# Kernel tuning notes

Measured on AMD Instinct MI355X. Metric: run time of the kernel, lower is better.

Reference implementation:

```python
import math
import jax, jax.numpy as jnp
import numpy as np

B, T, C, H = 4, 2048, 1024, 16
D = C // H  # head dim = 64


def setup_inputs() -> dict:
    key = jax.random.key(0)
    ks = jax.random.split(key, 9)
    s = 1.0 / math.sqrt(C)
    return {
        "x": jax.random.normal(ks[0], (B, T, C), jnp.float32),
        "Wq": jax.random.normal(ks[1], (C, C), jnp.float32) * s,
        "bq": jax.random.normal(ks[2], (C,), jnp.float32) * 0.02,
        "Wk": jax.random.normal(ks[3], (C, C), jnp.float32) * s,
        "bk": jax.random.normal(ks[4], (C,), jnp.float32) * 0.02,
        "Wv": jax.random.normal(ks[5], (C, C), jnp.float32) * s,
        "bv": jax.random.normal(ks[6], (C,), jnp.float32) * 0.02,
        "Wo": jax.random.normal(ks[7], (C, C), jnp.float32) * s,
        "bo": jax.random.normal(ks[8], (C,), jnp.float32) * 0.02,
    }


def reference(x, Wq, bq, Wk, bk, Wv, bv, Wo, bo):
    # Projections: (B,T,C) -> (B,H,T,D)
    def heads(y):
        return y.reshape(B, T, H, D).transpose(0, 2, 1, 3)

    q = heads(x @ Wq + bq)
    k = heads(x @ Wk + bk)
    v = heads(x @ Wv + bv)

    scale = 1.0 / math.sqrt(D)
    scores = jnp.einsum("bhqd,bhkd->bhqk", q, k) * scale  # (B,H,T,T)
    causal = jnp.tril(jnp.ones((T, T), dtype=bool))
    scores = jnp.where(causal[None, None], scores, jnp.float32(-jnp.inf))
    att = jax.nn.softmax(scores, axis=-1)

    y = jnp.einsum("bhqk,bhkd->bhqd", att, v)  # (B,H,T,D)
    y = y.transpose(0, 2, 1, 3).reshape(B, T, C)
    return y @ Wo + bo
```

## Files before the change

kernel.cpp:

```cpp
#include <hip/hip_runtime.h>

#define B_ 4
#define T_ 2048
#define C_ 1024
#define H_ 16
#define D_ 64
#define M_ (B_*T_)
#define CR3 3072

typedef unsigned short u16;
typedef __attribute__((ext_vector_type(8))) short short8;
typedef __attribute__((ext_vector_type(8))) unsigned short ushort8_t;
typedef __attribute__((ext_vector_type(4))) unsigned short ushort4_t;
typedef __attribute__((ext_vector_type(4))) float floatx4;
typedef __attribute__((ext_vector_type(16))) float f32x16;
typedef __attribute__((ext_vector_type(4))) unsigned int uint4_t;

__device__ __forceinline__ u16 f2bf(float f) {
  union { float f; unsigned u; } v; v.f = f;
  unsigned r = v.u + 0x7fffu + ((v.u >> 16) & 1u);
  return (u16)(r >> 16);
}

__device__ __forceinline__ void gload16(const void* g, void* l) {
  __builtin_amdgcn_global_load_lds((__attribute__((address_space(1))) void*)(g),
                                   (__attribute__((address_space(3))) void*)(l),
                                   16, 0, 0);
}

__device__ __forceinline__ unsigned cvtpk(float lo, float hi) {
  unsigned r;
  asm("v_cvt_pk_bf16_f32 %0, %1, %2" : "=v"(r) : "v"(lo), "v"(hi));
  return r;
}

__device__ __forceinline__ void pl32swap(unsigned &a, unsigned &b) {
  asm volatile("v_permlane32_swap_b32 %0, %1" : "+v"(a), "+v"(b));
}

#define MFMA32(a, b, c) __builtin_amdgcn_mfma_f32_32x32x16_bf16(a, b, c, 0, 0, 0)
#define MFMA16(a, b, c) __builtin_amdgcn_mfma_f32_16x16x32_bf16(a, b, c, 0, 0, 0)

__global__ __launch_bounds__(256) void convx_k(const float* __restrict__ x,
                                               u16* __restrict__ o) {
  int i = (blockIdx.x * 256 + threadIdx.x) * 4;
  floatx4 v = *(const floatx4*)(x + i);
  ushort4_t r;
#pragma unroll
  for (int j = 0; j < 4; ++j) r[j] = f2bf(v[j]);
  *(ushort4_t*)(o + i) = r;
}

__global__ __launch_bounds__(256) void wconv_k(const float* __restrict__ W0,
                                               const float* __restrict__ W1,
                                               const float* __restrict__ W2,
                                               const float* __restrict__ W3,
                                               u16* __restrict__ WT) {
  __shared__ float tile[64][65];
  const float* W = blockIdx.z == 0 ? W0 : blockIdx.z == 1 ? W1 : blockIdx.z == 2 ? W2 : W3;
  const float sc = blockIdx.z == 0 ? 0.125f * 1.44269504f : 1.0f;
  u16* Wt = WT + (size_t)blockIdx.z * (C_ * C_);
  int k0 = blockIdx.x * 64, n0 = blockIdx.y * 64;
  int t = threadIdx.x;
  int r = t >> 2, c0 = (t & 3) * 16;
#pragma unroll
  for (int j = 0; j < 4; ++j) {
    floatx4 v = *(const floatx4*)(W + (size_t)(k0 + r) * C_ + n0 + c0 + j * 4);
#pragma unroll
    for (int jj = 0; jj < 4; ++jj) tile[r][c0 + j * 4 + jj] = v[jj];
  }
  __syncthreads();
  ushort8_t o0, o1;
#pragma unroll
  for (int j = 0; j < 8; ++j) o0[j] = f2bf(tile[c0 + j][r] * sc);
#pragma unroll
  for (int j = 0; j < 8; ++j) o1[j] = f2bf(tile[c0 + 8 + j][r] * sc);
  *(ushort8_t*)(Wt + (size_t)(n0 + r) * C_ + k0 + c0) = o0;
  *(ushort8_t*)(Wt + (size_t)(n0 + r) * C_ + k0 + c0 + 8) = o1;
}

__global__ __launch_bounds__(256, 2) void gemm8_k(const u16* __restrict__ A,
                                                  const u16* __restrict__ Wt,
                                                  const float* __restrict__ b0,
                                                  const float* __restrict__ b1,
                                                  const float* __restrict__ b2,
                                                  float bsc0,
                                                  u16* __restrict__ Cout) {
  __shared__ u16 lds3[36864];
  const int tid = threadIdx.x;
  const int lane = tid & 63, wn = tid >> 6;
  const int l15 = lane & 15, g = lane >> 4;

  const int bid = blockIdx.x;
  const int swz = (bid & 7) * 96 + (bid >> 3);
  const int bn = swz >> 6, bm = swz & 63;
  const int m0 = bm * 128, n0 = bn * 256;

  const int srow = tid >> 2;
  const int scol = ((tid & 3) ^ ((srow >> 1) & 3)) * 8;
  const u16* gA = A  + (size_t)(m0 + srow) * 1024 + scol;
  const u16* gB = Wt + (size_t)(n0 + srow) * 1024 + scol;

#define STAGE(KT) do { \
    u16* s_ = lds3 + ((KT) % 3) * 12288; \
    gload16(gA + (KT) * 32,                      s_ + tid * 8); \
    gload16(gA + (size_t)64 * 1024 + (KT) * 32,  s_ + 2048 + tid * 8); \
    gload16(gB + (KT) * 32,                      s_ + 4096 + tid * 8); \
    gload16(gB + (size_t)64 * 1024 + (KT) * 32,  s_ + 6144 + tid * 8); \
    gload16(gB + (size_t)128 * 1024 + (KT) * 32, s_ + 8192 + tid * 8); \
    gload16(gB + (size_t)192 * 1024 + (KT) * 32, s_ + 10240 + tid * 8); \
  } while (0)

  floatx4 acc[8][4] = {};

  STAGE(0);
  STAGE(1);

  for (int kt = 0; kt < 32; ++kt) {
    if (kt < 31) asm volatile("s_waitcnt vmcnt(6)" ::: "memory");
    else         asm volatile("s_waitcnt vmcnt(0)" ::: "memory");
    __builtin_amdgcn_s_barrier();
    __builtin_amdgcn_sched_barrier(0);
    if (kt < 30) STAGE(kt + 2);

    const u16* Ab = lds3 + (kt % 3) * 12288;
    const u16* Bb = Ab + 4096;
    short8 af[8], bf[4];
#pragma unroll
    for (int mi = 0; mi < 8; ++mi) {
      int ra = mi * 16 + l15;
      af[mi] = *(const short8*)(Ab + ra * 32 + ((g ^ ((ra >> 1) & 3)) << 3));
    }
#pragma unroll
    for (int ni = 0; ni < 4; ++ni) {
      int rb = wn * 64 + ni * 16 + l15;
      bf[ni] = *(const short8*)(Bb + rb * 32 + ((g ^ ((rb >> 1) & 3)) << 3));
    }
    __builtin_amdgcn_s_setprio(1);
#pragma unroll
    for (int mi = 0; mi < 8; ++mi)
#pragma unroll
      for (int ni = 0; ni < 4; ++ni)
        acc[mi][ni] = MFMA16(af[mi], bf[ni], acc[mi][ni]);
    __builtin_amdgcn_s_setprio(0);
  }

#pragma unroll
  for (int mi = 0; mi < 8; ++mi) {
    int row = m0 + mi * 16 + g * 4;
#pragma unroll
    for (int ni = 0; ni < 4; ++ni) {
      int col = n0 + wn * 64 + ni * 16 + l15;
      int seg = col >> 10;
      const float* bp = seg == 0 ? b0 : seg == 1 ? b1 : b2;
      float bv = bp[col & 1023] * (seg == 0 ? bsc0 : 1.0f);
#pragma unroll
      for (int i = 0; i < 4; ++i)
        Cout[(size_t)(row + i) * CR3 + col] = f2bf(acc[mi][ni][i] + bv);
    }
  }
}

template <int OUTF32>
__global__ __launch_bounds__(256, 2) void gemm_k(const u16* __restrict__ A,
                                                 int astride,
                                                 const u16* __restrict__ Wt,
                                                 const float* __restrict__ b0,
                                                 void* __restrict__ Cout, int ostride) {
  __shared__ u16 As[128 * 32];
  __shared__ u16 Bs[128 * 32];
  const int tid = threadIdx.x;
  const int w = tid >> 6, lane = tid & 63;
  const int wr = (w >> 1) * 64, wc = (w & 1) * 64;
  const int l15 = lane & 15, g = lane >> 4;
  const int m0 = blockIdx.x * 128, n0 = blockIdx.y * 128;

  floatx4 acc[4][4] = {};

  const int srow = tid >> 2;
  const int scol = ((tid & 3) ^ ((srow >> 1) & 3)) * 8;
  const u16* ga = A + (size_t)(m0 + srow) * astride + scol;
  const u16* gb = Wt + (size_t)(n0 + srow) * C_ + scol;
  u16* lA = As + tid * 8;
  u16* lB = Bs + tid * 8;

  for (int kt = 0; kt < C_; kt += 32) {
    gload16(ga + kt, lA);
    gload16(ga + kt + (size_t)64 * astride, lA + 64 * 32);
    gload16(gb + kt, lB);
    gload16(gb + kt + (size_t)64 * C_, lB + 64 * 32);
    asm volatile("s_waitcnt vmcnt(0)" ::: "memory");
    __syncthreads();
    short8 af[4], bf[4];
#pragma unroll
    for (int i = 0; i < 4; ++i) {
      int ra = wr + i * 16 + l15;
      af[i] = *(const short8*)(As + ra * 32 + ((g ^ ((ra >> 1) & 3)) << 3));
    }
#pragma unroll
    for (int i = 0; i < 4; ++i) {
      int rb = wc + i * 16 + l15;
      bf[i] = *(const short8*)(Bs + rb * 32 + ((g ^ ((rb >> 1) & 3)) << 3));
    }
#pragma unroll
    for (int mi = 0; mi < 4; ++mi)
#pragma unroll
      for (int ni = 0; ni < 4; ++ni)
        acc[mi][ni] = MFMA16(af[mi], bf[ni], acc[mi][ni]);
    __syncthreads();
  }
#pragma unroll
  for (int mi = 0; mi < 4; ++mi) {
    int row = m0 + wr + mi * 16 + g * 4;
#pragma unroll
    for (int ni = 0; ni < 4; ++ni) {
      int col = n0 + wc + ni * 16 + l15;
      float bv = b0[col];
#pragma unroll
      for (int i = 0; i < 4; ++i) {
        float v = acc[mi][ni][i] + bv;
        if (OUTF32)
          ((float*)Cout)[(size_t)(row + i) * ostride + col] = v;
        else
          ((u16*)Cout)[(size_t)(row + i) * ostride + col] = f2bf(v);
      }
    }
  }
}

__global__ __launch_bounds__(256, 2) void attn_k(const u16* __restrict__ QKV,
                                                 u16* __restrict__ Yg) {
  __shared__ u16 Ks[2][64 * 64];
  __shared__ u16 Vt[2][64 * 64];

  const int tid = threadIdx.x;
  const int w = tid >> 6, lane = tid & 63;
  const int qi = lane & 31, h = lane >> 5;

  const int lid = blockIdx.x;
  const int a4 = lid >> 6;
  const int gq = a4 >> 2, iq = a4 & 3;
  const int jt = gq == 0 ? 15 - 2 * iq : gq == 1 ? 2 * iq : gq == 2 ? 14 - 2 * iq : 1 + 2 * iq;
  const int bh = lid & 63;
  const int nt = 2 * jt + 2;

  const size_t baseQ = (size_t)(bh >> 4) * T_ * CR3 + (size_t)(bh & 15) * D_;
  const size_t baseY = (size_t)(bh >> 4) * T_ * C_ + (size_t)(bh & 15) * D_;
  const u16* Kg = QKV + baseQ + 1024;
  const u16* Vg = QKV + baseQ + 2048;

  const int srow = tid >> 3, schunk = tid & 7;
  const int sgcol = (schunk ^ (srow & 7)) * 8;
  const u16* Kgr = Kg + (size_t)srow * CR3 + sgcol;
  const u16* Vgr = Vg + (size_t)srow * CR3 + schunk * 8;

  const int qw0 = 128 * jt + 32 * w;
  const int q_abs = qw0 + qi;

  short8 qf0, qf1, qf2, qf3;
  {
    const u16* Qr = QKV + baseQ + (size_t)q_abs * CR3 + 8 * h;
    qf0 = *(const short8*)(Qr);      qf1 = *(const short8*)(Qr + 16);
    qf2 = *(const short8*)(Qr + 32); qf3 = *(const short8*)(Qr + 48);
  }

  ushort8_t va, vbr;
  gload16(Kgr, &Ks[0][tid * 8]);
  gload16(Kgr + (size_t)32 * CR3, &Ks[0][2048 + tid * 8]);
  va = *(const ushort8_t*)(Vgr);
  vbr = *(const ushort8_t*)(Vgr + (size_t)32 * CR3);

  f32x16 y0 = {}, y1 = {};
  float l_run = 0.f;
  const float M0 = 13.0f;

  for (int t = 0; t < nt; ++t) {
    const int kv0 = t * 64;
    u16* Kb = Ks[t & 1];
    u16* Vb = Vt[t & 1];
    asm volatile("s_waitcnt vmcnt(0)" ::: "memory");
    {
      char* vbp = (char*)Vb;
#pragma unroll
      for (int j = 0; j < 8; ++j) {
        int d = schunk * 8 + j;
        int sl = ((schunk ^ j) & 7) << 4;
        *(u16*)(vbp + d * 128 + ((2 * srow) ^ sl)) = va[j];
        *(u16*)(vbp + d * 128 + ((2 * (srow + 32)) ^ sl)) = vbr[j];
      }
    }
    __syncthreads();
    if (t + 1 < nt) {
      int nkv = (t + 1) * 64;
      u16* dst = Ks[(t + 1) & 1];
      gload16(Kgr + (size_t)nkv * CR3, dst + tid * 8);
      gload16(Kgr + (size_t)(nkv + 32) * CR3, dst + 2048 + tid * 8);
      va = *(const ushort8_t*)(Vgr + (size_t)nkv * CR3);
      vbr = *(const ushort8_t*)(Vgr + (size_t)(nkv + 32) * CR3);
    }

    if (kv0 <= qw0 + 31) {
      f32x16 s0 = {}, s1 = {};
      {
        const int swq = (qi & 7) << 4;
        const char* kr0 = (const char*)Kb + qi * 128;
        const char* kr1 = (const char*)Kb + (qi + 32) * 128;
        short8 k0, k1;
        k0 = *(const short8*)(kr0 + ((16 * h) ^ swq));
        k1 = *(const short8*)(kr1 + ((16 * h) ^ swq));
        s0 = MFMA32(k0, qf0, s0); s1 = MFMA32(k1, qf0, s1);
        k0 = *(const short8*)(kr0 + ((32 + 16 * h) ^ swq));
        k1 = *(const short8*)(kr1 + ((32 + 16 * h) ^ swq));
        s0 = MFMA32(k0, qf1, s0); s1 = MFMA32(k1, qf1, s1);
        k0 = *(const short8*)(kr0 + ((64 + 16 * h) ^ swq));
        k1 = *(const short8*)(kr1 + ((64 + 16 * h) ^ swq));
        s0 = MFMA32(k0, qf2, s0); s1 = MFMA32(k1, qf2, s1);
        k0 = *(const short8*)(kr0 + ((96 + 16 * h) ^ swq));
        k1 = *(const short8*)(kr1 + ((96 + 16 * h) ^ swq));
        s0 = MFMA32(k0, qf3, s0); s1 = MFMA32(k1, qf3, s1);
      }
      if (kv0 + 63 > qw0) {
#pragma unroll
        for (int r = 0; r < 16; ++r) {
          int kvq = (r & 3) + 8 * (r >> 2) + 4 * h;
          if (kv0 + kvq > q_abs) s0[r] = -1e30f;
          if (kv0 + 32 + kvq > q_abs) s1[r] = -1e30f;
        }
      }
#pragma unroll
      for (int r = 0; r < 16; ++r) s0[r] = __builtin_amdgcn_exp2f(s0[r] - M0);
#pragma unroll
      for (int r = 0; r < 16; ++r) s1[r] = __builtin_amdgcn_exp2f(s1[r] - M0);
      {
        float a8[8];
#pragma unroll
        for (int r = 0; r < 8; ++r) a8[r] = (s0[r] + s0[r + 8]) + (s1[r] + s1[r + 8]);
#pragma unroll
        for (int r = 0; r < 4; ++r) a8[r] += a8[r + 4];
        l_run += (a8[0] + a8[1]) + (a8[2] + a8[3]);
      }
      unsigned pw[16];
      {
        unsigned a0, b0, a1, b1;
        a0 = cvtpk(s0[0], s0[1]);  b0 = cvtpk(s0[4], s0[5]);  pl32swap(a0, b0);
        a1 = cvtpk(s0[2], s0[3]);  b1 = cvtpk(s0[6], s0[7]);  pl32swap(a1, b1);
        pw[0] = a0; pw[1] = a1; pw[2] = b0; pw[3] = b1;
        a0 = cvtpk(s0[8], s0[9]);  b0 = cvtpk(s0[12], s0[13]); pl32swap(a0, b0);
        a1 = cvtpk(s0[10], s0[11]); b1 = cvtpk(s0[14], s0[15]); pl32swap(a1, b1);
        pw[4] = a0; pw[5] = a1; pw[6] = b0; pw[7] = b1;
        a0 = cvtpk(s1[0], s1[1]);  b0 = cvtpk(s1[4], s1[5]);  pl32swap(a0, b0);
        a1 = cvtpk(s1[2], s1[3]);  b1 = cvtpk(s1[6], s1[7]);  pl32swap(a1, b1);
        pw[8] = a0; pw[9] = a1; pw[10] = b0; pw[11] = b1;
        a0 = cvtpk(s1[8], s1[9]);  b0 = cvtpk(s1[12], s1[13]); pl32swap(a0, b0);
        a1 = cvtpk(s1[10], s1[11]); b1 = cvtpk(s1[14], s1[15]); pl32swap(a1, b1);
        pw[12] = a0; pw[13] = a1; pw[14] = b0; pw[15] = b1;
      }
      {
        const char* vb0 = (const char*)Vb + qi * 128;
        const char* vb1 = (const char*)Vb + (qi + 32) * 128;
        const int sx0 = (((qi >> 3) ^ qi) & 7) << 4;
        const int sx1 = sx0 ^ 0x40;
#pragma unroll
        for (int c = 0; c < 4; ++c) {
          int cb = 32 * c + 16 * h;
          uint4_t pt = {pw[c * 4 + 0], pw[c * 4 + 1], pw[c * 4 + 2], pw[c * 4 + 3]};
          short8 pa = __builtin_bit_cast(short8, pt);
          short8 v0 = *(const short8*)(vb0 + (cb ^ sx0));
          short8 v1 = *(const short8*)(vb1 + (cb ^ sx1));
          y0 = MFMA32(pa, v0, y0);
          y1 = MFMA32(pa, v1, y1);
        }
      }
    }
    __syncthreads();
  }

  l_run += __shfl_xor(l_run, 32);
  float linv = 1.0f / l_run;
#pragma unroll
  for (int r = 0; r < 16; ++r) {
    int qp = (r & 3) + 8 * (r >> 2) + 4 * h;
    float lv = __shfl(linv, qp);
    size_t row = baseY + (size_t)(qw0 + qp) * C_;
    Yg[row + qi] = f2bf(y0[r] * lv);
    Yg[row + 32 + qi] = f2bf(y1[r] * lv);
  }
}

extern "C" void kernel_launch(void* const* d_in, const int* in_sizes, int n_in,
                              void* d_out, int out_size, void* d_ws, size_t ws_size,
                              hipStream_t stream) {
  const float* x  = (const float*)d_in[0];
  const float* Wq = (const float*)d_in[1];
  const float* bq = (const float*)d_in[2];
  const float* Wk = (const float*)d_in[3];
  const float* bk = (const float*)d_in[4];
  const float* Wv = (const float*)d_in[5];
  const float* bv = (const float*)d_in[6];
  const float* Wo = (const float*)d_in[7];
  const float* bo = (const float*)d_in[8];
  float* out = (float*)d_out;

  char* ws = (char*)d_ws;
  u16* xb   = (u16*)ws;
  u16* WT   = (u16*)(ws + (size_t)16777216);
  u16* QKVb = (u16*)(ws + (size_t)25165824);
  u16* Yb = xb;

  convx_k<<<dim3(M_ * C_ / 1024), 256, 0, stream>>>(x, xb);
  wconv_k<<<dim3(16, 16, 4), 256, 0, stream>>>(Wq, Wk, Wv, Wo, WT);
  gemm8_k<<<dim3(768), 256, 0, stream>>>(xb, WT, bq, bk, bv, 0.125f * 1.44269504f, QKVb);
  attn_k<<<dim3(1024), 256, 0, stream>>>(QKVb, Yb);
  gemm_k<1><<<dim3(64, 8), 256, 0, stream>>>(Yb, C_, WT + (size_t)3 * 1048576, bo, out, C_);
}
```

Before: 164.2 us.

## Pre-transpose V globally and stream K/V from registers without shared memory

Adds a kernel that writes V transposed per head into the workspace. The attention kernel then drops LDS staging and barriers: each wave loads its own K and V fragments straight from global memory into registers, double-buffered in two register sets. Each wave handles two balanced 32-query tiles (j and 63-j), so causal work per wave is even, and the output is written into the V slot of the QKV buffer, which the final projection reads. This removes LDS traffic and __syncthreads overhead, but adds an extra transpose pass and redundant global/L2 reads, since every wave reloads K/V on its own.

```diff
diff --git a/kernel.cpp b/kernel.cpp
--- a/kernel.cpp
+++ b/kernel.cpp
@@ -159,6 +159,26 @@
         Cout[(size_t)(row + i) * CR3 + col] = f2bf(acc[mi][ni][i] + bv);
     }
   }
+}
+
+__global__ __launch_bounds__(256) void vt_k(const u16* __restrict__ QKV,
+                                            u16* __restrict__ Vtg) {
+  __shared__ unsigned tl[64][65];
+  const int tid = threadIdx.x;
+  const int bx = blockIdx.x, by = blockIdx.y;
+  const int r = tid >> 3, c8 = (tid & 7) * 8;
+  const size_t inb = ((size_t)(by >> 4) * T_ + (size_t)bx * 64) * CR3 + 2048 + (by & 15) * 64 + c8;
+  ushort8_t va = *(const ushort8_t*)(QKV + inb + (size_t)r * CR3);
+  ushort8_t vb = *(const ushort8_t*)(QKV + inb + (size_t)(r + 32) * CR3);
+#pragma unroll
+  for (int j = 0; j < 8; ++j) { tl[r][c8 + j] = va[j]; tl[r + 32][c8 + j] = vb[j]; }
+  __syncthreads();
+  ushort8_t o0, o1;
+#pragma unroll
+  for (int j = 0; j < 8; ++j) { o0[j] = (u16)tl[c8 + j][r]; o1[j] = (u16)tl[c8 + j][r + 32]; }
+  const size_t ob = ((size_t)by * 64 + r) * 2048 + bx * 64 + c8;
+  *(ushort8_t*)(Vtg + ob) = o0;
+  *(ushort8_t*)(Vtg + ob + (size_t)32 * 2048) = o1;
 }
 
 template <int OUTF32>
@@ -228,162 +248,110 @@
   }
 }
 
-__global__ __launch_bounds__(256, 2) void attn_k(const u16* __restrict__ QKV,
-                                                 u16* __restrict__ Yg) {
-  __shared__ u16 Ks[2][64 * 64];
-  __shared__ u16 Vt[2][64 * 64];
-
+__global__ __launch_bounds__(256, 2) void attn_k(u16* __restrict__ QKV,
+                                                 const u16* __restrict__ Vtg) {
   const int tid = threadIdx.x;
   const int w = tid >> 6, lane = tid & 63;
   const int qi = lane & 31, h = lane >> 5;
 
-  const int lid = blockIdx.x;
-  const int a4 = lid >> 6;
-  const int gq = a4 >> 2, iq = a4 & 3;
-  const int jt = gq == 0 ? 15 - 2 * iq : gq == 1 ? 2 * iq : gq == 2 ? 14 - 2 * iq : 1 + 2 * iq;
-  const int bh = lid & 63;
-  const int nt = 2 * jt + 2;
+  const int b = blockIdx.x;
+  const int bh = (b & 7) * 8 + ((b >> 3) & 7);
+  const int p = (b >> 6) * 4 + w;
 
   const size_t baseQ = (size_t)(bh >> 4) * T_ * CR3 + (size_t)(bh & 15) * D_;
-  const size_t baseY = (size_t)(bh >> 4) * T_ * C_ + (size_t)(bh & 15) * D_;
-  const u16* Kg = QKV + baseQ + 1024;
-  const u16* Vg = QKV + baseQ + 2048;
-
-  const int srow = tid >> 3, schunk = tid & 7;
-  const int sgcol = (schunk ^ (srow & 7)) * 8;
-  const u16* Kgr = Kg + (size_t)srow * CR3 + sgcol;
-  const u16* Vgr = Vg + (size_t)srow * CR3 + schunk * 8;
-
-  const int qw0 = 128 * jt + 32 * w;
-  const int q_abs = qw0 + qi;
+  const u16* Kl = QKV + baseQ + 1024 + (size_t)qi * CR3 + h * 8;
+  const u16* Vl = Vtg + (size_t)bh * (64 * 2048) + (size_t)qi * 2048 + h * 8;
 
   short8 qf0, qf1, qf2, qf3;
-  {
-    const u16* Qr = QKV + baseQ + (size_t)q_abs * CR3 + 8 * h;
-    qf0 = *(const short8*)(Qr);      qf1 = *(const short8*)(Qr + 16);
-    qf2 = *(const short8*)(Qr + 32); qf3 = *(const short8*)(Qr + 48);
-  }
-
-  ushort8_t va, vbr;
-  gload16(Kgr, &Ks[0][tid * 8]);
-  gload16(Kgr + (size_t)32 * CR3, &Ks[0][2048 + tid * 8]);
-  va = *(const ushort8_t*)(Vgr);
-  vbr = *(const ushort8_t*)(Vgr + (size_t)32 * CR3);
-
-  f32x16 y0 = {}, y1 = {};
-  float l_run = 0.f;
-  const float M0 = 13.0f;
-
-  for (int t = 0; t < nt; ++t) {
-    const int kv0 = t * 64;
-    u16* Kb = Ks[t & 1];
-    u16* Vb = Vt[t & 1];
-    asm volatile("s_waitcnt vmcnt(0)" ::: "memory");
+  short8 kA0, kA1, kA2, kA3, vA0, vA1, vA2, vA3;
+  short8 kB0, kB1, kB2, kB3, vB0, vB1, vB2, vB3;
+  f32x16 y0, y1;
+  float l_run;
+
+#define PRE(S, T) do { \
+    const u16* kp_ = Kl + (size_t)(T) * 32 * CR3; \
+    k##S##0 = *(const short8*)(kp_); \
+    k##S##1 = *(const short8*)(kp_ + 16); \
+    k##S##2 = *(const short8*)(kp_ + 32); \
+    k##S##3 = *(const short8*)(kp_ + 48); \
+    const u16* vp_ = Vl + (T) * 32; \
+    v##S##0 = *(const short8*)(vp_); \
+    v##S##1 = *(const short8*)(vp_ + 16); \
+    v##S##2 = *(const short8*)(vp_ + (size_t)32 * 2048); \
+    v##S##3 = *(const short8*)(vp_ + (size_t)32 * 2048 + 16); \
+  } while (0)
+
+#define COMP(S, KV0, DIAG) do { \
+    f32x16 s = {}; \
+    s = MFMA32(k##S##0, qf0, s); \
+    s = MFMA32(k##S##1, qf1, s); \
+    s = MFMA32(k##S##2, qf2, s); \
+    s = MFMA32(k##S##3, qf3, s); \
+    if (DIAG) { \
+      _Pragma("unroll") for (int r = 0; r < 16; ++r) { \
+        int kvq_ = (r & 3) + 8 * (r >> 2) + 4 * h; \
+        if ((KV0) + kvq_ > q_abs) s[r] = -1e30f; \
+      } \
+    } \
+    _Pragma("unroll") for (int r = 0; r < 16; ++r) s[r] = __builtin_amdgcn_exp2f(s[r] - 13.0f); \
+    { float a8_[8]; \
+      _Pragma("unroll") for (int r = 0; r < 8; ++r) a8_[r] = s[r] + s[r + 8]; \
+      _Pragma("unroll") for (int r = 0; r < 4; ++r) a8_[r] += a8_[r + 4]; \
+      l_run += (a8_[0] + a8_[1]) + (a8_[2] + a8_[3]); } \
+    unsigned pw_[8]; \
+    { unsigned a0_, b0_, a1_, b1_; \
+      a0_ = cvtpk(s[0], s[1]);  b0_ = cvtpk(s[4], s[5]);  pl32swap(a0_, b0_); \
+      a1_ = cvtpk(s[2], s[3]);  b1_ = cvtpk(s[6], s[7]);  pl32swap(a1_, b1_); \
+      pw_[0] = a0_; pw_[1] = a1_; pw_[2] = b0_; pw_[3] = b1_; \
+      a0_ = cvtpk(s[8], s[9]);  b0_ = cvtpk(s[12], s[13]); pl32swap(a0_, b0_); \
+      a1_ = cvtpk(s[10], s[11]); b1_ = cvtpk(s[14], s[15]); pl32swap(a1_, b1_); \
+      pw_[4] = a0_; pw_[5] = a1_; pw_[6] = b0_; pw_[7] = b1_; } \
+    { uint4_t p0_ = {pw_[0], pw_[1], pw_[2], pw_[3]}; \
+      uint4_t p1_ = {pw_[4], pw_[5], pw_[6], pw_[7]}; \
+      short8 pa0_ = __builtin_bit_cast(short8, p0_); \
+      short8 pa1_ = __builtin_bit_cast(short8, p1_); \
+      y0 = MFMA32(pa0_, v##S##0, y0); \
+      y0 = MFMA32(pa1_, v##S##1, y0); \
+      y1 = MFMA32(pa0_, v##S##2, y1); \
+      y1 = MFMA32(pa1_, v##S##3, y1); } \
+  } while (0)
+
+  for (int ph = 0; ph < 2; ++ph) {
+    const int j = ph ? (63 - p) : p;
+    const int ntt = j + 1;
+    const int qw0 = 32 * j;
+    const int q_abs = qw0 + qi;
     {
-      char* vbp = (char*)Vb;
-#pragma unroll
-      for (int j = 0; j < 8; ++j) {
-        int d = schunk * 8 + j;
-        int sl = ((schunk ^ j) & 7) << 4;
-        *(u16*)(vbp + d * 128 + ((2 * srow) ^ sl)) = va[j];
-        *(u16*)(vbp + d * 128 + ((2 * (srow + 32)) ^ sl)) = vbr[j];
+      const u16* Qr = QKV + baseQ + (size_t)q_abs * CR3 + 8 * h;
+      qf0 = *(const short8*)(Qr);      qf1 = *(const short8*)(Qr + 16);
+      qf2 = *(const short8*)(Qr + 32); qf3 = *(const short8*)(Qr + 48);
+    }
+    y0 = (f32x16){};
+    y1 = (f32x16){};
+    l_run = 0.f;
+
+    PRE(A, 0);
+    if (ntt > 1) PRE(B, 1);
+    for (int t = 0; t < ntt; t += 2) {
+      COMP(A, t * 32, t == j);
+      if (t + 2 < ntt) PRE(A, t + 2);
+      if (t + 1 < ntt) {
+        COMP(B, (t + 1) * 32, t + 1 == j);
+        if (t + 3 < ntt) PRE(B, t + 3);
       }
     }
-    __syncthreads();
-    if (t + 1 < nt) {
-      int nkv = (t + 1) * 64;
-      u16* dst = Ks[(t + 1) & 1];
-      gload16(Kgr + (size_t)nkv * CR3, dst + tid * 8);
-      gload16(Kgr + (size_t)(nkv + 32) * CR3, dst + 2048 + tid * 8);
-      va = *(const ushort8_t*)(Vgr + (size_t)nkv * CR3);
-      vbr = *(const ushort8_t*)(Vgr + (size_t)(nkv + 32) * CR3);
-    }
-
-    if (kv0 <= qw0 + 31) {
-      f32x16 s0 = {}, s1 = {};
-      {
-        const int swq = (qi & 7) << 4;
-        const char* kr0 = (const char*)Kb + qi * 128;
-        const char* kr1 = (const char*)Kb + (qi + 32) * 128;
-        short8 k0, k1;
-        k0 = *(const short8*)(kr0 + ((16 * h) ^ swq));
-        k1 = *(const short8*)(kr1 + ((16 * h) ^ swq));
-        s0 = MFMA32(k0, qf0, s0); s1 = MFMA32(k1, qf0, s1);
-        k0 = *(const short8*)(kr0 + ((32 + 16 * h) ^ swq));
-        k1 = *(const short8*)(kr1 + ((32 + 16 * h) ^ swq));
-        s0 = MFMA32(k0, qf1, s0); s1 = MFMA32(k1, qf1, s1);
-        k0 = *(const short8*)(kr0 + ((64 + 16 * h) ^ swq));
-        k1 = *(const short8*)(kr1 + ((64 + 16 * h) ^ swq));
-        s0 = MFMA32(k0, qf2, s0); s1 = MFMA32(k1, qf2, s1);
-        k0 = *(const short8*)(kr0 + ((96 + 16 * h) ^ swq));
-        k1 = *(const short8*)(kr1 + ((96 + 16 * h) ^ swq));
-        s0 = MFMA32(k0, qf3, s0); s1 = MFMA32(k1, qf3, s1);
-      }
-      if (kv0 + 63 > qw0) {
-#pragma unroll
-        for (int r = 0; r < 16; ++r) {
-          int kvq = (r & 3) + 8 * (r >> 2) + 4 * h;
-          if (kv0 + kvq > q_abs) s0[r] = -1e30f;
-          if (kv0 + 32 + kvq > q_abs) s1[r] = -1e30f;
-        }
-      }
-#pragma unroll
-      for (int r = 0; r < 16; ++r) s0[r] = __builtin_amdgcn_exp2f(s0[r] - M0);
-#pragma unroll
-      for (int r = 0; r < 16; ++r) s1[r] = __builtin_amdgcn_exp2f(s1[r] - M0);
-      {
-        float a8[8];
-#pragma unroll
-        for (int r = 0; r < 8; ++r) a8[r] = (s0[r] + s0[r + 8]) + (s1[r] + s1[r + 8]);
-#pragma unroll
-        for (int r = 0; r < 4; ++r) a8[r] += a8[r + 4];
-        l_run += (a8[0] + a8[1]) + (a8[2] + a8[3]);
-      }
-      unsigned pw[16];
-      {
-        unsigned a0, b0, a1, b1;
-        a0 = cvtpk(s0[0], s0[1]);  b0 = cvtpk(s0[4], s0[5]);  pl32swap(a0, b0);
-        a1 = cvtpk(s0[2], s0[3]);  b1 = cvtpk(s0[6], s0[7]);  pl32swap(a1, b1);
-        pw[0] = a0; pw[1] = a1; pw[2] = b0; pw[3] = b1;
-        a0 = cvtpk(s0[8], s0[9]);  b0 = cvtpk(s0[12], s0[13]); pl32swap(a0, b0);
-        a1 = cvtpk(s0[10], s0[11]); b1 = cvtpk(s0[14], s0[15]); pl32swap(a1, b1);
-        pw[4] = a0; pw[5] = a1; pw[6] = b0; pw[7] = b1;
-        a0 = cvtpk(s1[0], s1[1]);  b0 = cvtpk(s1[4], s1[5]);  pl32swap(a0, b0);
-        a1 = cvtpk(s1[2], s1[3]);  b1 = cvtpk(s1[6], s1[7]);  pl32swap(a1, b1);
-        pw[8] = a0; pw[9] = a1; pw[10] = b0; pw[11] = b1;
-        a0 = cvtpk(s1[8], s1[9]);  b0 = cvtpk(s1[12], s1[13]); pl32swap(a0, b0);
-        a1 = cvtpk(s1[10], s1[11]); b1 = cvtpk(s1[14], s1[15]); pl32swap(a1, b1);
-        pw[12] = a0; pw[13] = a1; pw[14] = b0; pw[15] = b1;
-      }
-      {
-        const char* vb0 = (const char*)Vb + qi * 128;
-        const char* vb1 = (const char*)Vb + (qi + 32) * 128;
-        const int sx0 = (((qi >> 3) ^ qi) & 7) << 4;
-        const int sx1 = sx0 ^ 0x40;
-#pragma unroll
-        for (int c = 0; c < 4; ++c) {
-          int cb = 32 * c + 16 * h;
-          uint4_t pt = {pw[c * 4 + 0], pw[c * 4 + 1], pw[c * 4 + 2], pw[c * 4 + 3]};
-          short8 pa = __builtin_bit_cast(short8, pt);
-          short8 v0 = *(const short8*)(vb0 + (cb ^ sx0));
-          short8 v1 = *(const short8*)(vb1 + (cb ^ sx1));
-          y0 = MFMA32(pa, v0, y0);
-          y1 = MFMA32(pa, v1, y1);
-        }
-      }
-    }
-    __syncthreads();
-  }
-
-  l_run += __shfl_xor(l_run, 32);
-  float linv = 1.0f / l_run;
-#pragma unroll
-  for (int r = 0; r < 16; ++r) {
-    int qp = (r & 3) + 8 * (r >> 2) + 4 * h;
-    float lv = __shfl(linv, qp);
-    size_t row = baseY + (size_t)(qw0 + qp) * C_;
-    Yg[row + qi] = f2bf(y0[r] * lv);
-    Yg[row + 32 + qi] = f2bf(y1[r] * lv);
+
+    l_run += __shfl_xor(l_run, 32);
+    float linv = 1.0f / l_run;
+    const size_t baseY = baseQ + 2048;
+#pragma unroll
+    for (int r = 0; r < 16; ++r) {
+      int qp = (r & 3) + 8 * (r >> 2) + 4 * h;
+      float lv = __shfl(linv, qp);
+      size_t row = baseY + (size_t)(qw0 + qp) * CR3;
+      QKV[row + qi] = f2bf(y0[r] * lv);
+      QKV[row + 32 + qi] = f2bf(y1[r] * lv);
+    }
   }
 }
 
@@ -405,11 +373,13 @@
   u16* xb   = (u16*)ws;
   u16* WT   = (u16*)(ws + (size_t)16777216);
   u16* QKVb = (u16*)(ws + (size_t)25165824);
-  u16* Yb = xb;
+  u16* Vtg  = xb;
 
   convx_k<<<dim3(M_ * C_ / 1024), 256, 0, stream>>>(x, xb);
   wconv_k<<<dim3(16, 16, 4), 256, 0, stream>>>(Wq, Wk, Wv, Wo, WT);
   gemm8_k<<<dim3(768), 256, 0, stream>>>(xb, WT, bq, bk, bv, 0.125f * 1.44269504f, QKVb);
-  attn_k<<<dim3(1024), 256, 0, stream>>>(QKVb, Yb);
-  gemm_k<1><<<dim3(64, 8), 256, 0, stream>>>(Yb, C_, WT + (size_t)3 * 1048576, bo, out, C_);
-}
+  vt_k<<<dim3(32, 64), 256, 0, stream>>>(QKVb, Vtg);
+  attn_k<<<dim3(512), 256, 0, stream>>>(QKVb, Vtg);
+  gemm_k<1><<<dim3(64, 8), 256, 0, stream>>>(QKVb + 2048, CR3, WT + (size_t)3 * 1048576,
+                                             bo, out, C_);
+}
```

After: 232.5 us. +41.6%, slower.
